# Kernel optimization log

Hardware: AMD Instinct MI355X
Metric: run time of the kernel (lower is better)

The kernel has to match this reference:

```python
import jax, jax.numpy as jnp
import numpy as np

N_FFT = 1024
HOP = 256
WIN = N_FFT  # win_length = n_fft in VocosISTFTHead
PAD = (WIN - HOP) // 2  # 384, 'same' padding trim
CLAMP_MAX = 100.0


def _hann_periodic(n):
    # matches torch.hann_window(n, periodic=True)
    return 0.5 * (1.0 - jnp.cos(2.0 * jnp.pi * jnp.arange(n, dtype=jnp.float32) / n))


def setup_inputs() -> dict:
    key = jax.random.key(0)
    k1, k2, k3 = jax.random.split(key, 3)
    B, T, H = 16, 2048, 512
    hidden_states = jax.random.normal(k1, (B, T, H), dtype=jnp.float32)
    # out_proj: Linear(hidden_dim, n_fft+2); scaled so exp(magnitude) stays sane
    W = jax.random.normal(k2, (N_FFT + 2, H), dtype=jnp.float32) * 0.02
    b = jax.random.normal(k3, (N_FFT + 2,), dtype=jnp.float32) * 0.02
    window = _hann_periodic(WIN)
    return {"hidden_states": hidden_states, "W": W, "b": b, "window": window}


def reference(hidden_states, W, b, window):
    B, T, _ = hidden_states.shape
    # linear projection -> [B, T, n_fft+2] -> transpose -> [B, n_fft+2, T]
    spec = (hidden_states @ W.T + b).transpose(0, 2, 1)
    half = (N_FFT + 2) // 2  # n_fft//2 + 1 = 513 freq bins
    magnitude = jnp.minimum(jnp.exp(spec[:, :half]), CLAMP_MAX)
    phase = spec[:, half:]
    coeffs = magnitude * (jnp.cos(phase) + 1j * jnp.sin(phase))  # [B, F, T] complex
    # inverse rfft along freq axis, norm='backward' (default) -> [B, n_fft, T]
    frames = jnp.fft.irfft(coeffs, n=N_FFT, axis=1)
    frames = frames * window[None, :, None]
    L = (T - 1) * HOP + WIN
    idx = (jnp.arange(T)[:, None] * HOP + jnp.arange(WIN)[None, :]).reshape(-1)
    frames_flat = frames.transpose(0, 2, 1).reshape(B, -1)
    audio = jnp.zeros((B, L), frames.dtype).at[:, idx].add(frames_flat)
    # NOLA normalization: overlap-added squared window
    wsq = jnp.broadcast_to(window ** 2, (T, WIN)).reshape(-1)
    norm = jnp.zeros((L,), window.dtype).at[idx].add(wsq)
    return audio[:, PAD:-PAD] / norm[PAD:-PAD]
```

## Files before the change

### kernel.cpp

```cpp
#include <hip/hip_runtime.h>
#include <hip/hip_fp16.h>
#include <math.h>
#include <stdint.h>


#define FRAMES  32768
#define TWO_PI  6.283185307179586f

typedef unsigned short ushort_t;
typedef __attribute__((ext_vector_type(8))) _Float16 f16x8;
typedef __attribute__((ext_vector_type(4))) float f32x4;

#define GLDS(gp, lp) __builtin_amdgcn_global_load_lds( \
    (const __attribute__((address_space(1))) void*)(gp), \
    (__attribute__((address_space(3))) void*)(lp), 16, 0, 0)

__device__ __forceinline__ float2 f2(float x, float y){ return make_float2(x,y); }
__device__ __forceinline__ float2 cadd(float2 a, float2 b){ return f2(a.x+b.x, a.y+b.y); }
__device__ __forceinline__ float2 csub(float2 a, float2 b){ return f2(a.x-b.x, a.y-b.y); }
__device__ __forceinline__ float2 cmul(float2 a, float2 b){ return f2(a.x*b.x - a.y*b.y, a.x*b.y + a.y*b.x); }

__device__ __forceinline__ uint32_t pack2h(float a, float b) {
  const ushort_t ha = __half_as_ushort(__float2half_rn(a));
  const ushort_t hb = __half_as_ushort(__float2half_rn(b));
  return (uint32_t)ha | ((uint32_t)hb << 16);
}

__global__ __launch_bounds__(256) void convert_AB(
    const float* __restrict__ hs, const float* __restrict__ Wm,
    const float* __restrict__ bias, ushort_t* __restrict__ Af,
    ushort_t* __restrict__ Whi, __half* __restrict__ coeffs)
{
  const int bid = blockIdx.x;
  const int t = threadIdx.x;
  if (bid < 2048) {
    const int r = t >> 4, c = t & 15;
    const int m = bid * 16 + r;
    const float* src = hs + (size_t)m * 512 + c * 32;
    const float* wm  = Wm + (size_t)512  * 512 + c * 32;
    const float* wp  = Wm + (size_t)1025 * 512 + c * 32;

    float v[32];
    #pragma unroll
    for (int i = 0; i < 8; ++i) *(float4*)&v[i*4] = *(const float4*)(src + i*4);

    float dm = 0.f, dp = 0.f;
    #pragma unroll
    for (int i = 0; i < 8; ++i) {
      const float4 a  = *(const float4*)&v[i*4];
      const float4 m4 = *(const float4*)(wm + i*4);
      const float4 p4 = *(const float4*)(wp + i*4);
      dm = fmaf(a.x,m4.x, fmaf(a.y,m4.y, fmaf(a.z,m4.z, fmaf(a.w,m4.w, dm))));
      dp = fmaf(a.x,p4.x, fmaf(a.y,p4.y, fmaf(a.z,p4.z, fmaf(a.w,p4.w, dp))));
    }

    uint32_t hu[16];
    #pragma unroll
    for (int i = 0; i < 16; ++i) hu[i] = pack2h(v[2*i], v[2*i+1]);
    ushort_t* dh = Af + (size_t)m * 512 + c * 32;
    #pragma unroll
    for (int q = 0; q < 4; ++q)
      *(uint4*)(dh + q*8) = make_uint4(hu[4*q], hu[4*q+1], hu[4*q+2], hu[4*q+3]);

    #pragma unroll
    for (int off = 8; off; off >>= 1) {
      dm += __shfl_xor(dm, off, 16);
      dp += __shfl_xor(dp, off, 16);
    }
    if (c == 0) {
      const float sm = dm + bias[512], sp = dp + bias[1025];
      const float mag = fminf(__expf(sm), 100.0f);
      coeffs[(size_t)m * 1024 + 1] = __float2half_rn(mag * __cosf(sp));
    }
  } else {
    const int gid = (bid - 2048) * 256 + t;
    const int sd = gid & 3;
    const int r  = (gid >> 2) & 255;
    const int kt = (gid >> 10) & 15;
    const int yb = gid >> 14;
    const int srow = (r < 128) ? (yb*128 + r) : (513 + yb*128 + (r - 128));
    const float* src = Wm + (size_t)srow * 512 + kt*32 + sd*8;
    const float4 a = *(const float4*)src;
    const float4 b = *(const float4*)(src + 4);
    const uint4 o = make_uint4(pack2h(a.x,a.y), pack2h(a.z,a.w),
                               pack2h(b.x,b.y), pack2h(b.z,b.w));
    *(uint4*)(Whi + (size_t)gid * 8) = o;
  }
}

__global__ __launch_bounds__(512, 2) void gemm_mfma(
    const ushort_t* __restrict__ Af, const ushort_t* __restrict__ Whi,
    const float* __restrict__ bias, __half* __restrict__ coeffs)
{
  __shared__ ushort_t Ab[24576];

  const int tid = threadIdx.x;
  const int w = tid >> 6, l = tid & 63;
  const int wr = w >> 2, wc = w & 3;
  const int lc = l & 15, kg = l >> 4;

  const int bid = blockIdx.x;
  const int swz = (bid & 7) * 64 + (bid >> 3);
  const int mb = swz >> 2, yb = swz & 3;

  uint32_t pa_off[2], lofs[2];
  #pragma unroll
  for (int ch = 0; ch < 2; ++ch) {
    const int g = ch*512 + tid;
    const int r = g >> 2, sd = g & 3;
    lofs[ch] = r*32 + sd*8;
    const int sl = sd ^ ((r >> 1) & 3);
    pa_off[ch] = (uint32_t)(mb*256 + r)*512 + sl*8;
  }
  uint32_t pb_off[4];
  #pragma unroll
  for (int cf = 0; cf < 4; ++cf) {
    const int rB = ((cf < 2) ? 0 : 128) + wc*32 + (cf & 1)*16 + lc;
    pb_off[cf] = (uint32_t)yb*131072u + rB*32 + kg*8;
  }

  f32x4 acc[8][4];
  #pragma unroll
  for (int rf = 0; rf < 8; ++rf)
    #pragma unroll
    for (int cf = 0; cf < 4; ++cf)
      #pragma unroll
      for (int q = 0; q < 4; ++q) acc[rf][cf][q] = 0.f;

  const int asl = (kg ^ ((lc >> 1) & 3)) * 8;

  f16x8 p[4], q[4];

#define WAITV2 asm volatile("s_waitcnt vmcnt(2) lgkmcnt(0)" ::: "memory")
#define WAITV0 asm volatile("s_waitcnt vmcnt(0) lgkmcnt(0)" ::: "memory")
#define SB     __builtin_amdgcn_s_barrier()
#define SCH0   __builtin_amdgcn_sched_barrier(0)

#define DSREAD(DST, BASE, RF0) do {                                      \
    _Pragma("unroll")                                                    \
    for (int r4 = 0; r4 < 4; ++r4) {                                     \
      const int rr = wr*128 + ((RF0) + r4)*16 + lc;                      \
      DST[r4] = *(const f16x8*)(&Ab[(BASE) + rr*32 + asl]);              \
    }                                                                    \
  } while (0)

#define MFMA16(FA, RF0, RB) do {                                         \
    __builtin_amdgcn_s_setprio(1);                                       \
    _Pragma("unroll")                                                    \
    for (int r4 = 0; r4 < 4; ++r4)                                       \
      _Pragma("unroll")                                                  \
      for (int cf = 0; cf < 4; ++cf)                                     \
        acc[(RF0)+r4][cf] = __builtin_amdgcn_mfma_f32_16x16x32_f16(      \
            FA[r4], RB[cf], acc[(RF0)+r4][cf], 0, 0, 0);                 \
    __builtin_amdgcn_s_setprio(0);                                       \
  } while (0)

#define ITER(KT, RBC, RBN, LAST) do {                                    \
    if (LAST) { WAITV0; } else { WAITV2; }                               \
    SB;                                                                  \
               \
    DSREAD(q, aR, 4);                                                    \
    if ((KT) < 14) GLDS(Af + pa_off[0] + ((KT)+2)*32, &Ab[aW + lofs[0]]);\
    if ((KT) < 15) {                                                     \
      RBN[0] = *(const f16x8*)(Whi + pb_off[0] + ((KT)+1)*8192);         \
      RBN[1] = *(const f16x8*)(Whi + pb_off[1] + ((KT)+1)*8192);         \
    }                                                                    \
    SCH0;                                                                \
    MFMA16(p, 0, RBC);                                                   \
     \
    if ((KT) < 15) DSREAD(p, aN, 0);                                     \
    if ((KT) < 14) GLDS(Af + pa_off[1] + ((KT)+2)*32, &Ab[aW + lofs[1]]);\
    if ((KT) < 15) {                                                     \
      RBN[2] = *(const f16x8*)(Whi + pb_off[2] + ((KT)+1)*8192);         \
      RBN[3] = *(const f16x8*)(Whi + pb_off[3] + ((KT)+1)*8192);         \
    }                                                                    \
    SCH0;                                                                \
    MFMA16(q, 4, RBC);                                                   \
    { const unsigned t_ = aR; aR = aN; aN = aW; aW = t_; }               \
  } while (0)

  f16x8 rb0[4], rb1[4];
  GLDS(Af + pa_off[0], &Ab[lofs[0]]);
  GLDS(Af + pa_off[1], &Ab[lofs[1]]);
  GLDS(Af + pa_off[0] + 32, &Ab[8192 + lofs[0]]);
  GLDS(Af + pa_off[1] + 32, &Ab[8192 + lofs[1]]);
  SCH0;
  #pragma unroll
  for (int j = 0; j < 4; ++j) rb0[j] = *(const f16x8*)(Whi + pb_off[j]);
  SCH0;
  asm volatile("s_waitcnt vmcnt(6)" ::: "memory");
  SB;
  unsigned aR = 0, aN = 8192, aW = 16384;
  DSREAD(p, aR, 0);

  for (int k2 = 0; k2 < 8; ++k2) {
    ITER(2*k2,     rb0, rb1, false);
    ITER(2*k2 + 1, rb1, rb0, k2 == 7);
  }
#undef ITER
#undef DSREAD
#undef MFMA16

  #pragma unroll
  for (int j = 0; j < 2; ++j) {
    const int pcol = yb*128 + wc*32 + j*16 + lc;
    const float bm = bias[pcol], bp = bias[513 + pcol];
    #pragma unroll
    for (int rf = 0; rf < 8; ++rf) {
      const int rbase = mb*256 + wr*128 + rf*16 + kg*4;
      #pragma unroll
      for (int qi = 0; qi < 4; ++qi) {
        const float sm = acc[rf][j][qi]   + bm;
        const float sp = acc[rf][2+j][qi] + bp;
        const float mag = fminf(__expf(sm), 100.0f);
        const float aa = mag * __cosf(sp);
        const float bb = mag * __sinf(sp);
        __half* row = coeffs + (size_t)(rbase + qi) * 1024;
        if (pcol == 0) row[0] = __float2half_rn(aa);
        else *(__half2*)(row + 2*pcol) = __float22half2_rn(make_float2(aa, bb));
      }
    }
  }
}

#define PIDX(s) ((s) + ((s) >> 3))

template<int NS>
__device__ __forceinline__ void stage_fft(const float2* in, float2* out, int l)
{
  float2 v[8];
  #pragma unroll
  for (int r = 0; r < 8; ++r) v[r] = in[PIDX(l + 64*r)];
  if (NS > 1) {
    const float ang = TWO_PI * (float)(l & (NS-1)) / (float)(NS * 8);
    float sn, cs; __sincosf(ang, &sn, &cs);
    const float2 wb = f2(cs, sn);
    float2 cur = wb;
    #pragma unroll
    for (int r = 1; r < 8; ++r) { v[r] = cmul(v[r], cur); cur = cmul(cur, wb); }
  }
  const float2 e0=v[0], e1=v[2], e2=v[4], e3=v[6];
  const float2 o0=v[1], o1=v[3], o2=v[5], o3=v[7];
  float2 a = cadd(e0,e2), b = csub(e0,e2), c = cadd(e1,e3), d = csub(e1,e3);
  const float2 E0 = cadd(a,c), E2 = csub(a,c);
  const float2 E1 = f2(b.x - d.y, b.y + d.x), E3 = f2(b.x + d.y, b.y - d.x);
  a = cadd(o0,o2); b = csub(o0,o2); c = cadd(o1,o3); d = csub(o1,o3);
  const float2 O0 = cadd(a,c), O2 = csub(a,c);
  const float2 O1 = f2(b.x - d.y, b.y + d.x), O3 = f2(b.x + d.y, b.y - d.x);
  const float r2 = 0.70710678118654752f;
  const float2 t0 = O0;
  const float2 t1 = f2(r2*(O1.x - O1.y),  r2*(O1.x + O1.y));
  const float2 t2 = f2(-O2.y, O2.x);
  const float2 t3 = f2(-r2*(O3.x + O3.y), r2*(O3.x - O3.y));
  float2 X[8];
  X[0]=cadd(E0,t0); X[4]=csub(E0,t0);
  X[1]=cadd(E1,t1); X[5]=csub(E1,t1);
  X[2]=cadd(E2,t2); X[6]=csub(E2,t2);
  X[3]=cadd(E3,t3); X[7]=csub(E3,t3);
  const int idxD = (l / NS) * (NS * 8) + (l & (NS-1));
  #pragma unroll
  for (int q = 0; q < 8; ++q) out[PIDX(idxD + q*NS)] = X[q];
}

__global__ __launch_bounds__(256) void fft_win(
    const __half* coeffs, __half* frames, const float* __restrict__ window)
{
  __shared__ float2 bA[4][576];
  __shared__ float2 bB[4][576];
  const int tid = threadIdx.x;
  const int w = tid >> 6, l = tid & 63;
  const size_t f = (size_t)blockIdx.x * 4 + w;
  const __half2* crow = (const __half2*)(coeffs + f * 1024);

  const float sc = 1.0f / 1024.0f;
  #pragma unroll
  for (int j = 0; j < 4; ++j) {
    const int k = 1 + l + 64*j;
    const float2 Ck = __half22float2(crow[k]);
    const float2 Cq = __half22float2(crow[512-k]);
    float sn, cs; __sincosf(TWO_PI * (1.0f/1024.0f) * (float)k, &sn, &cs);
    const float Ex = sc*(Ck.x + Cq.x), Ey = sc*(Ck.y - Cq.y);
    const float Dx = Ck.x - Cq.x,      Dy = Ck.y + Cq.y;
    const float Ox = sc*(cs*Dx - sn*Dy), Oy = sc*(cs*Dy + sn*Dx);
    bA[w][PIDX(k)]     = f2(Ex - Oy, Ey + Ox);
    bA[w][PIDX(512-k)] = f2(Ex + Oy, Ox - Ey);
  }
  if (l == 0) {
    const float2 dn = __half22float2(crow[0]);
    bA[w][PIDX(0)] = f2(sc*(dn.x + dn.y), sc*(dn.x - dn.y));
  }
  __syncthreads();
  stage_fft<1 >(bA[w], bB[w], l);
  __syncthreads();
  stage_fft<8 >(bB[w], bA[w], l);
  __syncthreads();
  stage_fft<64>(bA[w], bB[w], l);
  __syncthreads();

  __half2* frow = (__half2*)(frames + f * 1024);
  #pragma unroll
  for (int j = 0; j < 8; ++j) {
    const int m = l + 64*j;
    const float2 z  = bB[w][PIDX(m)];
    const float2 wv = *(const float2*)(window + 2*m);
    frow[m] = __float22half2_rn(make_float2(z.x * wv.x, z.y * wv.y));
  }
}

__global__ __launch_bounds__(256) void gather_out(
    const __half* __restrict__ frames, const float* __restrict__ window,
    float* __restrict__ out)
{
  const int idx = blockIdx.x * 256 + threadIdx.x;
  const int b  = idx >> 19;
  const int jj = idx & 524287;
  const int s  = jj + 384;
  int tlo = (s - 768) >> 8; if (tlo < 0) tlo = 0;
  int thi = s >> 8;         if (thi > 2047) thi = 2047;
  float acc = 0.f, nrm = 0.f;
  for (int t = tlo; t <= thi; ++t) {
    const int n = s - (t << 8);
    const float wv = window[n];
    nrm = fmaf(wv, wv, nrm);
    acc += __half2float(frames[(size_t)(b * 2048 + t) * 1024 + n]);
  }
  out[idx] = acc / nrm;
}

extern "C" void kernel_launch(void* const* d_in, const int* in_sizes, int n_in,
                              void* d_out, int out_size, void* d_ws, size_t ws_size,
                              hipStream_t stream)
{
  const float* hs     = (const float*)d_in[0];
  const float* Wm     = (const float*)d_in[1];
  const float* bias   = (const float*)d_in[2];
  const float* window = (const float*)d_in[3];

  char* base = (char*)d_ws;
  ushort_t* Af     = (ushort_t*)base;
  ushort_t* Whi    = (ushort_t*)(base + 33554432);
  __half*   frames = (__half*)base;
  __half*   coeffs = (__half*)(base + 67108864);

  convert_AB<<<2304, 256, 0, stream>>>(hs, Wm, bias, Af, Whi, coeffs);
  gemm_mfma<<<512,  512, 0, stream>>>(Af, Whi, bias, coeffs);
  fft_win<<<FRAMES / 4, 256, 0, stream>>>(coeffs, frames, window);
  gather_out<<<8388608 / 256, 256, 0, stream>>>(frames, window, (float*)d_out);
}
```

Before: 150.1 us.

## Vectorize overlap-add gather, use wave barriers in FFT, simplify GEMM epilogue

The overlap-add gather kernel now makes each thread produce four consecutive output samples, using 8-byte half loads, float4 window loads and a float4 store. This cuts the thread count by four and widens memory transactions. The FFT kernel replaces block-wide __syncthreads with wave barriers, since each wave owns its own LDS row buffers. The GEMM epilogue is reorganized to hoist bias loads and drop the pcol==0 check from the second column. The wave-barrier change is only correct if each frame's FFT is processed entirely within one wavefront, and that relies on wavefront-wide LDS ordering.

```diff
diff --git a/kernel.cpp b/kernel.cpp
--- a/kernel.cpp
+++ b/kernel.cpp
@@ -201,29 +201,39 @@
 #undef DSREAD
 #undef MFMA16
 
-  #pragma unroll
-  for (int j = 0; j < 2; ++j) {
-    const int pcol = yb*128 + wc*32 + j*16 + lc;
-    const float bm = bias[pcol], bp = bias[513 + pcol];
-    #pragma unroll
-    for (int rf = 0; rf < 8; ++rf) {
-      const int rbase = mb*256 + wr*128 + rf*16 + kg*4;
-      #pragma unroll
-      for (int qi = 0; qi < 4; ++qi) {
-        const float sm = acc[rf][j][qi]   + bm;
-        const float sp = acc[rf][2+j][qi] + bp;
+  const int pc0 = yb*128 + wc*32 + lc;
+  const int pc1 = pc0 + 16;
+  const float bm0 = bias[pc0], bp0 = bias[513 + pc0];
+  const float bm1 = bias[pc1], bp1 = bias[513 + pc1];
+  #pragma unroll
+  for (int rf = 0; rf < 8; ++rf) {
+    const int rbase = mb*256 + wr*128 + rf*16 + kg*4;
+    #pragma unroll
+    for (int qi = 0; qi < 4; ++qi) {
+      __half* row = coeffs + (size_t)(rbase + qi) * 1024;
+      {
+        const float sm = acc[rf][0][qi] + bm0;
+        const float sp = acc[rf][2][qi] + bp0;
         const float mag = fminf(__expf(sm), 100.0f);
         const float aa = mag * __cosf(sp);
         const float bb = mag * __sinf(sp);
-        __half* row = coeffs + (size_t)(rbase + qi) * 1024;
-        if (pcol == 0) row[0] = __float2half_rn(aa);
-        else *(__half2*)(row + 2*pcol) = __float22half2_rn(make_float2(aa, bb));
+        if (pc0 == 0) row[0] = __float2half_rn(aa);
+        else *(__half2*)(row + 2*pc0) = __float22half2_rn(make_float2(aa, bb));
+      }
+      {
+        const float sm = acc[rf][1][qi] + bm1;
+        const float sp = acc[rf][3][qi] + bp1;
+        const float mag = fminf(__expf(sm), 100.0f);
+        const float aa = mag * __cosf(sp);
+        const float bb = mag * __sinf(sp);
+        *(__half2*)(row + 2*pc1) = __float22half2_rn(make_float2(aa, bb));
       }
     }
   }
 }
 
 #define PIDX(s) ((s) + ((s) >> 3))
+#define WFENCE  __builtin_amdgcn_wave_barrier()
 
 template<int NS>
 __device__ __forceinline__ void stage_fft(const float2* in, float2* out, int l)
@@ -289,13 +299,13 @@
     const float2 dn = __half22float2(crow[0]);
     bA[w][PIDX(0)] = f2(sc*(dn.x + dn.y), sc*(dn.x - dn.y));
   }
-  __syncthreads();
+  WFENCE;
   stage_fft<1 >(bA[w], bB[w], l);
-  __syncthreads();
+  WFENCE;
   stage_fft<8 >(bB[w], bA[w], l);
-  __syncthreads();
+  WFENCE;
   stage_fft<64>(bA[w], bB[w], l);
-  __syncthreads();
+  WFENCE;
 
   __half2* frow = (__half2*)(frames + f * 1024);
   #pragma unroll
@@ -312,19 +322,25 @@
     float* __restrict__ out)
 {
   const int idx = blockIdx.x * 256 + threadIdx.x;
-  const int b  = idx >> 19;
-  const int jj = idx & 524287;
-  const int s  = jj + 384;
+  const int b  = idx >> 17;
+  const int g  = idx & 131071;
+  const int s  = g * 4 + 384;
   int tlo = (s - 768) >> 8; if (tlo < 0) tlo = 0;
   int thi = s >> 8;         if (thi > 2047) thi = 2047;
-  float acc = 0.f, nrm = 0.f;
+  float a0=0.f, a1=0.f, a2=0.f, a3=0.f;
+  float n0=0.f, n1=0.f, n2=0.f, n3=0.f;
+  const __half* fb = frames + (size_t)b * 2048 * 1024;
   for (int t = tlo; t <= thi; ++t) {
     const int n = s - (t << 8);
-    const float wv = window[n];
-    nrm = fmaf(wv, wv, nrm);
-    acc += __half2float(frames[(size_t)(b * 2048 + t) * 1024 + n]);
-  }
-  out[idx] = acc / nrm;
+    const float4 wv = *(const float4*)(window + n);
+    const uint2 fr = *(const uint2*)(fb + (size_t)t * 1024 + n);
+    const float2 f01 = __half22float2(*(const __half2*)&fr.x);
+    const float2 f23 = __half22float2(*(const __half2*)&fr.y);
+    a0 += f01.x; a1 += f01.y; a2 += f23.x; a3 += f23.y;
+    n0 = fmaf(wv.x, wv.x, n0); n1 = fmaf(wv.y, wv.y, n1);
+    n2 = fmaf(wv.z, wv.z, n2); n3 = fmaf(wv.w, wv.w, n3);
+  }
+  *(float4*)(out + (size_t)idx * 4) = make_float4(a0/n0, a1/n1, a2/n2, a3/n3);
 }
 
 extern "C" void kernel_launch(void* const* d_in, const int* in_sizes, int n_in,
@@ -345,5 +361,5 @@
   convert_AB<<<2304, 256, 0, stream>>>(hs, Wm, bias, Af, Whi, coeffs);
   gemm_mfma<<<512,  512, 0, stream>>>(Af, Whi, bias, coeffs);
   fft_win<<<FRAMES / 4, 256, 0, stream>>>(coeffs, frames, window);
-  gather_out<<<8388608 / 256, 256, 0, stream>>>(frames, window, (float*)d_out);
-}
+  gather_out<<<8192, 256, 0, stream>>>(frames, window, (float*)d_out);
+}
```

After: 134.2 us. -10.6%, faster.
